# Optimization experiments

Measured on AMD Instinct MI355X. Metric: run time of the kernel, lower is better.

Reference implementation:

```python
import jax, jax.numpy as jnp
import numpy as np

N_NODES = 100000
N_EDGES = 1600000
IN_F = 64
OUT_F = 32
NEG_SLOPE = 0.2


def setup_inputs() -> dict:
    key = jax.random.key(0)
    k = jax.random.split(key, 6)
    x = jax.random.normal(k[0], (N_NODES, IN_F), dtype=jnp.float32)
    edge_index = jax.random.randint(k[1], (2, N_EDGES), 0, N_NODES, dtype=jnp.int64)
    W = jax.random.normal(k[2], (IN_F, OUT_F), dtype=jnp.float32) * 0.1
    att_src = jax.random.normal(k[3], (OUT_F,), dtype=jnp.float32) * 0.1
    att_dst = jax.random.normal(k[4], (OUT_F,), dtype=jnp.float32) * 0.1
    bias = jax.random.normal(k[5], (OUT_F,), dtype=jnp.float32) * 0.1
    return {"x": x, "edge_index": edge_index, "W": W,
            "att_src": att_src, "att_dst": att_dst, "bias": bias}


def reference(x, edge_index, W, att_src, att_dst, bias):
    N = x.shape[0]
    # Linear projection (single head, concat=True -> [N, OUT_F])
    h = x @ W  # [N, C]
    a_src = h @ att_src  # [N] per-node source attention logit contribution
    a_dst = h @ att_dst  # [N] per-node destination contribution
    # add self loops (PyG GATConv default add_self_loops=True)
    loop = jnp.arange(N, dtype=edge_index.dtype)
    src = jnp.concatenate([edge_index[0], loop])  # [E+N] message senders
    dst = jnp.concatenate([edge_index[1], loop])  # [E+N] message receivers
    # attention logits per edge, LeakyReLU(alpha_src[j] + alpha_dst[i])
    e = jax.nn.leaky_relu(a_src[src] + a_dst[dst], NEG_SLOPE)
    # segment softmax over incoming edges of each destination node
    m = jax.ops.segment_max(e, dst, num_segments=N)  # every node has a self loop
    ex = jnp.exp(e - m[dst])
    denom = jax.ops.segment_sum(ex, dst, num_segments=N)
    alpha = ex / denom[dst]  # [E+N]
    # weighted scatter-add of source features into destinations
    out = jax.ops.segment_sum(h[src] * alpha[:, None], dst, num_segments=N)
    out = out + bias
    # GATLayer activation='relu'
    return jax.nn.relu(out)
```

## Files before the change

### kernel.cpp

```cpp
#include <hip/hip_runtime.h>
#include <hip/hip_fp16.h>
#include <math.h>

#define IN_F 64
#define OUT_F 32
#define NEG_SLOPE 0.2f

#define BK_SHIFT 6
#define BK 64
#define NBMAX 2048
#define NBLKA 256
#define CAPSHIFT 11
#define CAP 2048
#define PSTAGE 4
#define COLCAP 2304

typedef _Float16 half8_t __attribute__((ext_vector_type(8)));
typedef float float4_t __attribute__((ext_vector_type(4)));
typedef int int4_t __attribute__((ext_vector_type(4)));


__device__ __forceinline__ float leaky(float v) {
    return (v > 0.0f) ? v : NEG_SLOPE * v;
}

__device__ __forceinline__ int incScan512(int v, int tid, int* wsum) {
    const int lane = tid & 63, wid = tid >> 6;
    #pragma unroll
    for (int m = 1; m < 64; m <<= 1) {
        int u = __shfl_up(v, m);
        if (lane >= m) v += u;
    }
    if (lane == 63) wsum[wid] = v;
    __syncthreads();
    int add = 0;
    for (int k = 0; k < wid; ++k) add += wsum[k];
    __syncthreads();
    return v + add;
}

__global__ __launch_bounds__(512) void k_zero(int* __restrict__ cursor,
                                              __half2* __restrict__ h2,
                                              float* __restrict__ asrc, int N) {
    const int tid = threadIdx.x;
    #pragma unroll
    for (int k = 0; k < NBMAX / 512; ++k) cursor[tid + k * 512] = 0;
    if (tid < 16) h2[(size_t)N * 16 + tid] = __floats2half2_rn(0.0f, 0.0f);
    if (tid == 16) asrc[N] = -1e30f;
}

__global__ __launch_bounds__(256) void k_projbpart(
        const float* __restrict__ x, const float* __restrict__ W,
        const float* __restrict__ att_src, const float* __restrict__ att_dst,
        __half2* __restrict__ h2, float* __restrict__ asrc, float* __restrict__ adst,
        const int* __restrict__ src, const int* __restrict__ dst,
        int* __restrict__ cursor, int* __restrict__ recs,
        int N, int NB, int E, int epb, int PB) {
    __shared__ int smem[2 * NBMAX];
    const int tid = threadIdx.x;

    if (blockIdx.x >= PB) {
        int* cnt  = smem;
        int* lcur = smem + NBMAX;
        const int blk = blockIdx.x - PB;
        for (int b = tid; b < NB; b += 256) cnt[b] = 0;
        __syncthreads();
        const int e0 = blk * epb, e1 = min(E, e0 + epb);
        for (int e = e0 + tid; e < e1; e += 256)
            atomicAdd(&cnt[dst[e] >> BK_SHIFT], 1);
        __syncthreads();
        const int off = (blk * 389) % NB;
        for (int i = tid; i < NB; i += 256) {
            int b = i + off; if (b >= NB) b -= NB;
            const int c = cnt[b];
            if (c > 0) lcur[b] = (b << CAPSHIFT) + atomicAdd(&cursor[b], c);
        }
        __syncthreads();
        for (int e = e0 + tid; e < e1; e += 256) {
            int s = src[e];
            int d = dst[e];
            int p = atomicAdd(&lcur[d >> BK_SHIFT], 1);
            recs[p] = ((d & (BK - 1)) << 17) | s;
        }
        return;
    }

    const int wv   = tid >> 6;
    const int lane = tid & 63;
    const int m    = lane & 15;
    const int quad = lane >> 4;
    const int node0 = (blockIdx.x * 4 + wv) * 16;
    if (node0 >= N) return;

    const int kb = quad * 8;
    half8_t b00, b01, b10, b11;
    #pragma unroll
    for (int j = 0; j < 8; ++j) {
        b00[j] = (_Float16)W[(kb + j) * OUT_F + m];
        b01[j] = (_Float16)W[(32 + kb + j) * OUT_F + m];
        b10[j] = (_Float16)W[(kb + j) * OUT_F + 16 + m];
        b11[j] = (_Float16)W[(32 + kb + j) * OUT_F + 16 + m];
    }
    const int row = min(node0 + m, N - 1);
    const float* xr = x + (size_t)row * IN_F + kb;
    float4_t xa = *(const float4_t*)(xr);
    float4_t xb = *(const float4_t*)(xr + 4);
    float4_t xc = *(const float4_t*)(xr + 32);
    float4_t xd = *(const float4_t*)(xr + 36);
    half8_t a0, a1;
    #pragma unroll
    for (int j = 0; j < 4; ++j) {
        a0[j] = (_Float16)xa[j]; a0[4 + j] = (_Float16)xb[j];
        a1[j] = (_Float16)xc[j]; a1[4 + j] = (_Float16)xd[j];
    }
    float4_t acc0 = {0.f, 0.f, 0.f, 0.f};
    float4_t acc1 = {0.f, 0.f, 0.f, 0.f};
    acc0 = __builtin_amdgcn_mfma_f32_16x16x32_f16(a0, b00, acc0, 0, 0, 0);
    acc0 = __builtin_amdgcn_mfma_f32_16x16x32_f16(a1, b01, acc0, 0, 0, 0);
    acc1 = __builtin_amdgcn_mfma_f32_16x16x32_f16(a0, b10, acc1, 0, 0, 0);
    acc1 = __builtin_amdgcn_mfma_f32_16x16x32_f16(a1, b11, acc1, 0, 0, 0);

    const float aS0 = att_src[m], aS1 = att_src[16 + m];
    const float aD0 = att_dst[m], aD1 = att_dst[16 + m];
    #pragma unroll
    for (int r = 0; r < 4; ++r) {
        const int node = node0 + quad * 4 + r;
        float h0 = acc0[r], h1 = acc1[r];
        float h0p = __shfl_xor(h0, 1);
        float h1p = __shfl_xor(h1, 1);
        if (node < N && (m & 1) == 0) {
            __half2 hv;
            hv.x = __float2half_rn(h0); hv.y = __float2half_rn(h0p);
            h2[(size_t)node * 16 + (m >> 1)] = hv;
            __half2 hw;
            hw.x = __float2half_rn(h1); hw.y = __float2half_rn(h1p);
            h2[(size_t)node * 16 + 8 + (m >> 1)] = hw;
        }
        float vs = h0 * aS0 + h1 * aS1;
        float vd = h0 * aD0 + h1 * aD1;
        #pragma unroll
        for (int mm = 1; mm < 16; mm <<= 1) {
            vs += __shfl_xor(vs, mm);
            vd += __shfl_xor(vd, mm);
        }
        if (node < N && m == 0) {
            asrc[node] = vs;
            adst[node] = vd;
        }
    }
}

__global__ __launch_bounds__(512) void k_pg(const int* __restrict__ recs,
                                            const int* __restrict__ cursor,
                                            const float* __restrict__ asrc,
                                            const float* __restrict__ adst,
                                            const __half2* __restrict__ h2,
                                            const float* __restrict__ bias,
                                            float* __restrict__ out,
                                            int NB, int E, int N) {
    __shared__ __align__(16) int colsh[COLCAP];
    __shared__ int fineCnt[BK];
    __shared__ int cur[BK];
    __shared__ int loff[BK];
    __shared__ int lpad[BK];
    __shared__ int wsum[8];
    const int b = blockIdx.x, tid = threadIdx.x;
    const int node0 = b << BK_SHIFT;

    const size_t cb0 = (size_t)b << CAPSHIFT;
    const int count = min(cursor[b], CAP);

    for (int i = tid; i < COLCAP; i += 512) colsh[i] = N;
    if (tid < BK) fineCnt[tid] = 0;
    __syncthreads();

    int myrec[PSTAGE];
    #pragma unroll
    for (int k = 0; k < PSTAGE; ++k) {
        int i = tid + k * 512;
        if (i < count) {
            int v = recs[cb0 + i];
            myrec[k] = v;
            atomicAdd(&fineCnt[v >> 17], 1);
        }
    }
    __syncthreads();

    const int v0 = (tid < BK) ? fineCnt[tid] : 0;
    const int pv = (v0 + 3) & ~3;
    const int vin = (tid < BK) ? pv : 0;
    const int pinc = incScan512(vin, tid, wsum);
    const int pexcl = pinc - vin;
    if (tid < BK) {
        loff[tid] = pexcl;
        lpad[tid] = pv;
        cur[tid]  = pexcl;
    }
    __syncthreads();

    #pragma unroll
    for (int k = 0; k < PSTAGE; ++k) {
        int i = tid + k * 512;
        if (i < count) {
            int r = myrec[k];
            int p = atomicAdd(&cur[r >> 17], 1);
            colsh[p] = r & 0x1FFFF;
        }
    }
    __syncthreads();

    const int wid  = tid >> 6;
    const int lane = tid & 63;
    const int g    = lane >> 4;
    const int c2   = lane & 15;
    for (int i = 0; i < 8; ++i) {
        const int dloc = wid * 8 + i;
        const int n = node0 + dloc;
        if (n >= N) break;
        const float adst_n = adst[n];
        float l = 0.0f, accx = 0.0f, accy = 0.0f;
        if (g == 0) {
            float p = __expf(leaky(asrc[n] + adst_n));
            float2 hv = __half22float2(h2[(size_t)n * 16 + c2]);
            l = p; accx = p * hv.x; accy = p * hv.y;
        }
        const int base = loff[dloc];
        const int nch  = lpad[dloc] >> 2;
        for (int c = g; c < nch; c += 4) {
            const int4_t cc = *(const int4_t*)(&colsh[base + c * 4]);
            const int s0 = cc[0], s1 = cc[1], s2 = cc[2], s3 = cc[3];
            float a0 = asrc[s0], a1 = asrc[s1], a2 = asrc[s2], a3 = asrc[s3];
            float2 h0 = __half22float2(h2[(size_t)s0 * 16 + c2]);
            float2 h1 = __half22float2(h2[(size_t)s1 * 16 + c2]);
            float2 hv2 = __half22float2(h2[(size_t)s2 * 16 + c2]);
            float2 h3 = __half22float2(h2[(size_t)s3 * 16 + c2]);
            float p0 = __expf(leaky(a0 + adst_n));
            float p1 = __expf(leaky(a1 + adst_n));
            float p2 = __expf(leaky(a2 + adst_n));
            float p3 = __expf(leaky(a3 + adst_n));
            l += (p0 + p1) + (p2 + p3);
            accx += p0 * h0.x + p1 * h1.x + p2 * hv2.x + p3 * h3.x;
            accy += p0 * h0.y + p1 * h1.y + p2 * hv2.y + p3 * h3.y;
        }
        l    += __shfl_xor(l, 16);    l    += __shfl_xor(l, 32);
        accx += __shfl_xor(accx, 16); accx += __shfl_xor(accx, 32);
        accy += __shfl_xor(accy, 16); accy += __shfl_xor(accy, 32);
        if (g == 0) {
            float inv = 1.0f / l;
            float2 bb = ((const float2*)bias)[c2];
            float2 o;
            o.x = fmaxf(accx * inv + bb.x, 0.0f);
            o.y = fmaxf(accy * inv + bb.y, 0.0f);
            ((float2*)out)[(size_t)n * 16 + c2] = o;
        }
    }
}

extern "C" void kernel_launch(void* const* d_in, const int* in_sizes, int n_in,
                              void* d_out, int out_size, void* d_ws, size_t ws_size,
                              hipStream_t stream) {
    const float* x        = (const float*)d_in[0];
    const int*   eidx     = (const int*)d_in[1];
    const float* W        = (const float*)d_in[2];
    const float* att_src  = (const float*)d_in[3];
    const float* att_dst  = (const float*)d_in[4];
    const float* bias     = (const float*)d_in[5];
    float* out = (float*)d_out;

    const int N = in_sizes[0] / IN_F;
    const int E = in_sizes[1] / 2;
    const int* src = eidx;
    const int* dst = eidx + E;

    const int NB  = (N + BK - 1) >> BK_SHIFT;
    const int epb = (E + NBLKA - 1) / NBLKA;

    int* u = (int*)d_ws;
    size_t o = 0;
    __half2* h2     = (__half2*)(u + o); o += (size_t)(N + 1) * 16;
    float*   asrc   = (float*)(u + o);   o += N + 1;
    float*   adst   = (float*)(u + o);   o += N;
    int*     cursor = u + o;             o += NBMAX;
    int*     recs   = u + o;             o += (size_t)NBMAX << CAPSHIFT;

    const int PB = (N + 63) / 64;

    k_zero<<<1, 512, 0, stream>>>(cursor, h2, asrc, N);
    k_projbpart<<<PB + NBLKA, 256, 0, stream>>>(x, W, att_src, att_dst,
                                                h2, asrc, adst, src, dst,
                                                cursor, recs, N, NB, E, epb, PB);
    k_pg<<<NB, 512, 0, stream>>>(recs, cursor, asrc, adst, h2, bias, out, NB, E, N);
}
```

Before: 154.4 us.

## Precompute edge attention weights during bucket scatter and enlarge projection/partition blocks

Moves the per-edge exp(leaky(asrc[s]+adst[d])) computation into the local scatter phase of the aggregation kernel, storing weights in a new shared-memory array. The gather loop then reads them from LDS instead of doing a second asrc gather plus exp. Destination logits are cached in shared memory. Separately, the projection/partition kernel moves from 256- to 1024-thread blocks, so each block handles more nodes or edges. This adds about 9KB of LDS per aggregation block, which may lower occupancy. The bigger blocks change atomic contention patterns in the partition phase.

```diff
diff --git a/kernel.cpp b/kernel.cpp
--- a/kernel.cpp
+++ b/kernel.cpp
@@ -49,7 +49,7 @@
     if (tid == 16) asrc[N] = -1e30f;
 }
 
-__global__ __launch_bounds__(256) void k_projbpart(
+__global__ __launch_bounds__(1024) void k_projbpart(
         const float* __restrict__ x, const float* __restrict__ W,
         const float* __restrict__ att_src, const float* __restrict__ att_dst,
         __half2* __restrict__ h2, float* __restrict__ asrc, float* __restrict__ adst,
@@ -63,20 +63,20 @@
         int* cnt  = smem;
         int* lcur = smem + NBMAX;
         const int blk = blockIdx.x - PB;
-        for (int b = tid; b < NB; b += 256) cnt[b] = 0;
+        for (int b = tid; b < NB; b += 1024) cnt[b] = 0;
         __syncthreads();
         const int e0 = blk * epb, e1 = min(E, e0 + epb);
-        for (int e = e0 + tid; e < e1; e += 256)
+        for (int e = e0 + tid; e < e1; e += 1024)
             atomicAdd(&cnt[dst[e] >> BK_SHIFT], 1);
         __syncthreads();
         const int off = (blk * 389) % NB;
-        for (int i = tid; i < NB; i += 256) {
+        for (int i = tid; i < NB; i += 1024) {
             int b = i + off; if (b >= NB) b -= NB;
             const int c = cnt[b];
             if (c > 0) lcur[b] = (b << CAPSHIFT) + atomicAdd(&cursor[b], c);
         }
         __syncthreads();
-        for (int e = e0 + tid; e < e1; e += 256) {
+        for (int e = e0 + tid; e < e1; e += 1024) {
             int s = src[e];
             int d = dst[e];
             int p = atomicAdd(&lcur[d >> BK_SHIFT], 1);
@@ -89,7 +89,7 @@
     const int lane = tid & 63;
     const int m    = lane & 15;
     const int quad = lane >> 4;
-    const int node0 = (blockIdx.x * 4 + wv) * 16;
+    const int node0 = (blockIdx.x * 16 + wv) * 16;
     if (node0 >= N) return;
 
     const int kb = quad * 8;
@@ -159,10 +159,12 @@
                                             float* __restrict__ out,
                                             int NB, int E, int N) {
     __shared__ __align__(16) int colsh[COLCAP];
+    __shared__ __align__(16) float pcol[COLCAP];
     __shared__ int fineCnt[BK];
     __shared__ int cur[BK];
     __shared__ int loff[BK];
     __shared__ int lpad[BK];
+    __shared__ float adl[BK];
     __shared__ int wsum[8];
     const int b = blockIdx.x, tid = threadIdx.x;
     const int node0 = b << BK_SHIFT;
@@ -170,8 +172,12 @@
     const size_t cb0 = (size_t)b << CAPSHIFT;
     const int count = min(cursor[b], CAP);
 
-    for (int i = tid; i < COLCAP; i += 512) colsh[i] = N;
-    if (tid < BK) fineCnt[tid] = 0;
+    for (int i = tid; i < COLCAP; i += 512) { colsh[i] = N; pcol[i] = 0.0f; }
+    if (tid < BK) {
+        fineCnt[tid] = 0;
+        const int n = node0 + tid;
+        adl[tid] = (n < N) ? adst[n] : 0.0f;
+    }
     __syncthreads();
 
     int myrec[PSTAGE];
@@ -203,8 +209,11 @@
         int i = tid + k * 512;
         if (i < count) {
             int r = myrec[k];
-            int p = atomicAdd(&cur[r >> 17], 1);
-            colsh[p] = r & 0x1FFFF;
+            int d = r >> 17;
+            int s = r & 0x1FFFF;
+            int p = atomicAdd(&cur[d], 1);
+            colsh[p] = s;
+            pcol[p] = __expf(leaky(asrc[s] + adl[d]));
         }
     }
     __syncthreads();
@@ -217,10 +226,9 @@
         const int dloc = wid * 8 + i;
         const int n = node0 + dloc;
         if (n >= N) break;
-        const float adst_n = adst[n];
         float l = 0.0f, accx = 0.0f, accy = 0.0f;
         if (g == 0) {
-            float p = __expf(leaky(asrc[n] + adst_n));
+            float p = __expf(leaky(asrc[n] + adl[dloc]));
             float2 hv = __half22float2(h2[(size_t)n * 16 + c2]);
             l = p; accx = p * hv.x; accy = p * hv.y;
         }
@@ -228,19 +236,15 @@
         const int nch  = lpad[dloc] >> 2;
         for (int c = g; c < nch; c += 4) {
             const int4_t cc = *(const int4_t*)(&colsh[base + c * 4]);
+            const float4_t pp = *(const float4_t*)(&pcol[base + c * 4]);
             const int s0 = cc[0], s1 = cc[1], s2 = cc[2], s3 = cc[3];
-            float a0 = asrc[s0], a1 = asrc[s1], a2 = asrc[s2], a3 = asrc[s3];
             float2 h0 = __half22float2(h2[(size_t)s0 * 16 + c2]);
             float2 h1 = __half22float2(h2[(size_t)s1 * 16 + c2]);
             float2 hv2 = __half22float2(h2[(size_t)s2 * 16 + c2]);
             float2 h3 = __half22float2(h2[(size_t)s3 * 16 + c2]);
-            float p0 = __expf(leaky(a0 + adst_n));
-            float p1 = __expf(leaky(a1 + adst_n));
-            float p2 = __expf(leaky(a2 + adst_n));
-            float p3 = __expf(leaky(a3 + adst_n));
-            l += (p0 + p1) + (p2 + p3);
-            accx += p0 * h0.x + p1 * h1.x + p2 * hv2.x + p3 * h3.x;
-            accy += p0 * h0.y + p1 * h1.y + p2 * hv2.y + p3 * h3.y;
+            l += (pp[0] + pp[1]) + (pp[2] + pp[3]);
+            accx += pp[0] * h0.x + pp[1] * h1.x + pp[2] * hv2.x + pp[3] * h3.x;
+            accy += pp[0] * h0.y + pp[1] * h1.y + pp[2] * hv2.y + pp[3] * h3.y;
         }
         l    += __shfl_xor(l, 16);    l    += __shfl_xor(l, 32);
         accx += __shfl_xor(accx, 16); accx += __shfl_xor(accx, 32);
@@ -283,11 +287,11 @@
     int*     cursor = u + o;             o += NBMAX;
     int*     recs   = u + o;             o += (size_t)NBMAX << CAPSHIFT;
 
-    const int PB = (N + 63) / 64;
+    const int PB = (N + 255) / 256;
 
     k_zero<<<1, 512, 0, stream>>>(cursor, h2, asrc, N);
-    k_projbpart<<<PB + NBLKA, 256, 0, stream>>>(x, W, att_src, att_dst,
-                                                h2, asrc, adst, src, dst,
-                                                cursor, recs, N, NB, E, epb, PB);
+    k_projbpart<<<PB + NBLKA, 1024, 0, stream>>>(x, W, att_src, att_dst,
+                                                 h2, asrc, adst, src, dst,
+                                                 cursor, recs, N, NB, E, epb, PB);
     k_pg<<<NB, 512, 0, stream>>>(recs, cursor, asrc, adst, h2, bias, out, NB, E, N);
 }
```

After: 147.7 us. 1.05x faster.
